# Kernel tuning notes

Measured on AMD Instinct MI355X. Metric: run time of the kernel, lower is better.

Reference implementation:

```python
import jax, jax.numpy as jnp
import numpy as np

D, HEADS, HD, L, P, DFF = 256, 8, 32, 4, 4, 2048
B, NQ = 4, 900
SHAPES = [(128, 128), (64, 64), (32, 32), (16, 16)]
S = sum(h * w for h, w in SHAPES)


def setup_inputs():
    ks = iter(jax.random.split(jax.random.key(0), 20))
    rn = lambda *s: jax.random.normal(next(ks), s, jnp.float32) * 0.02
    cxcy = jax.random.uniform(next(ks), (B, NQ, 1, 2), minval=0.1, maxval=0.9)
    wh = jax.random.uniform(next(ks), (B, NQ, 1, 2), minval=0.05, maxval=0.3)
    ref = jnp.broadcast_to(jnp.concatenate([cxcy, wh], -1), (B, NQ, L, 4))
    starts = np.cumsum([0] + [h * w for h, w in SHAPES[:-1]])
    return dict(
        query=jax.random.normal(next(ks), (B, NQ, D), jnp.float32),
        query_pos=jax.random.normal(next(ks), (B, NQ, D), jnp.float32),
        reference_points=ref,
        input_flatten=jax.random.normal(next(ks), (B, S, D), jnp.float32),
        input_spatial_shapes=jnp.array(SHAPES, jnp.int32),
        input_level_start_index=jnp.array(starts, jnp.int32),
        sa_in_w=rn(3, D, D), sa_in_b=jnp.zeros((3, D)),
        sa_out_w=rn(D, D), sa_out_b=jnp.zeros((D,)),
        norm1_g=jnp.ones((D,)), norm1_b=jnp.zeros((D,)),
        value_w=rn(D, D), value_b=jnp.zeros((D,)),
        off_w=rn(D, HEADS * L * P * 2),
        off_b=jax.random.uniform(next(ks), (HEADS * L * P * 2,), minval=-1.0, maxval=1.0),
        aw_w=rn(D, HEADS * L * P), aw_b=jnp.zeros((HEADS * L * P,)),
        ca_out_w=rn(D, D), ca_out_b=jnp.zeros((D,)),
        norm2_g=jnp.ones((D,)), norm2_b=jnp.zeros((D,)),
        lin1_w=rn(D, DFF), lin1_b=jnp.zeros((DFF,)),
        lin2_w=rn(DFF, D), lin2_b=jnp.zeros((D,)),
        norm3_g=jnp.ones((D,)), norm3_b=jnp.zeros((D,)),
    )


def _ln(x, g, b, eps=1e-5):
    m = x.mean(-1, keepdims=True)
    v = ((x - m) ** 2).mean(-1, keepdims=True)
    return (x - m) * jax.lax.rsqrt(v + eps) * g + b


def _msdeform(q, input_flatten, ref, shapes, starts, value_w, value_b,
              off_w, off_b, aw_w, aw_b, out_w, out_b):
    Bq, Nq, _ = q.shape
    # value: (B, heads, S, head_dim)
    v = (input_flatten @ value_w + value_b).reshape(Bq, -1, HEADS, HD).transpose(0, 2, 1, 3)
    off = (q @ off_w + off_b).reshape(Bq, Nq, HEADS, L, P, 2).transpose(0, 2, 1, 3, 4, 5)
    aw = jax.nn.softmax((q @ aw_w + aw_b).reshape(Bq, Nq, HEADS, L * P), axis=-1)
    aw = aw.reshape(Bq, Nq, HEADS, L, P).transpose(0, 2, 1, 3, 4)  # (B,H,Nq,L,P)
    refc = ref[:, None, :, :, None, :]  # (B,1,Nq,L,1,4)
    # box refs: center + offset/P * wh * 0.5  (Deformable-DETR convention)
    loc = refc[..., :2] + off / P * refc[..., 2:] * 0.5  # (B,H,Nq,L,P,2)
    out = jnp.zeros((Bq, HEADS, Nq, HD), q.dtype)
    for l, (H, W) in enumerate(shapes):
        vl = jax.lax.dynamic_slice_in_dim(v, starts[l], H * W, axis=2)  # (B,H,HW,hd)
        x = loc[:, :, :, l, :, 0] * W - 0.5  # align_corners=False pixel coords
        y = loc[:, :, :, l, :, 1] * H - 0.5
        x0, y0 = jnp.floor(x), jnp.floor(y)
        dx, dy = x - x0, y - y0

        def g(xi, yi):
            valid = (xi >= 0) & (xi < W) & (yi >= 0) & (yi < H)  # zero padding
            idx = (jnp.clip(yi, 0, H - 1) * W + jnp.clip(xi, 0, W - 1)).astype(jnp.int32)
            gat = jnp.take_along_axis(vl, idx.reshape(Bq, HEADS, Nq * P, 1), axis=2)
            return gat.reshape(Bq, HEADS, Nq, P, HD) * valid[..., None]

        samp = (((1 - dx) * (1 - dy))[..., None] * g(x0, y0)
                + (dx * (1 - dy))[..., None] * g(x0 + 1, y0)
                + ((1 - dx) * dy)[..., None] * g(x0, y0 + 1)
                + (dx * dy)[..., None] * g(x0 + 1, y0 + 1))
        out = out + jnp.sum(aw[:, :, :, l, :, None] * samp, axis=3)
    return out.transpose(0, 2, 1, 3).reshape(Bq, Nq, D) @ out_w + out_b


def _layer(query, query_pos, reference_points, input_flatten, shapes, starts, p):
    Bq, Nq, _ = query.shape
    qk = query + query_pos
    heads = lambda x: x.reshape(Bq, Nq, HEADS, HD).transpose(0, 2, 1, 3)
    qh = heads(qk @ p['sa_in_w'][0] + p['sa_in_b'][0])
    kh = heads(qk @ p['sa_in_w'][1] + p['sa_in_b'][1])
    vh = heads(query @ p['sa_in_w'][2] + p['sa_in_b'][2])
    attn = jax.nn.softmax(jnp.einsum('bhqd,bhkd->bhqk', qh, kh) * (HD ** -0.5), axis=-1)
    sa = jnp.einsum('bhqk,bhkd->bhqd', attn, vh).transpose(0, 2, 1, 3).reshape(Bq, Nq, D)
    sa = sa @ p['sa_out_w'] + p['sa_out_b']
    x = _ln(query + sa, p['norm1_g'], p['norm1_b'])
    ca = _msdeform(x + query_pos, input_flatten, reference_points, shapes, starts,
                   p['value_w'], p['value_b'], p['off_w'], p['off_b'],
                   p['aw_w'], p['aw_b'], p['ca_out_w'], p['ca_out_b'])
    x = _ln(x + ca, p['norm2_g'], p['norm2_b'])
    ffn = jax.nn.relu(x @ p['lin1_w'] + p['lin1_b']) @ p['lin2_w'] + p['lin2_b']
    return _ln(x + ffn, p['norm3_g'], p['norm3_b'])


PNAMES = ['sa_in_w', 'sa_in_b', 'sa_out_w', 'sa_out_b', 'norm1_g', 'norm1_b',
          'value_w', 'value_b', 'off_w', 'off_b', 'aw_w', 'aw_b',
          'ca_out_w', 'ca_out_b', 'norm2_g', 'norm2_b',
          'lin1_w', 'lin1_b', 'lin2_w', 'lin2_b', 'norm3_g', 'norm3_b']


def reference(query, query_pos, reference_points, input_flatten,
              input_spatial_shapes, input_level_start_index,
              sa_in_w, sa_in_b, sa_out_w, sa_out_b, norm1_g, norm1_b,
              value_w, value_b, off_w, off_b, aw_w, aw_b,
              ca_out_w, ca_out_b, norm2_g, norm2_b,
              lin1_w, lin1_b, lin2_w, lin2_b, norm3_g, norm3_b):
    # spatial shapes / start indices are static structural metadata
    shapes = [(int(h), int(w)) for h, w in np.asarray(input_spatial_shapes)]
    starts = [int(s) for s in np.asarray(input_level_start_index)]
    p = dict(zip(PNAMES, (sa_in_w, sa_in_b, sa_out_w, sa_out_b, norm1_g, norm1_b,
                          value_w, value_b, off_w, off_b, aw_w, aw_b,
                          ca_out_w, ca_out_b, norm2_g, norm2_b,
                          lin1_w, lin1_b, lin2_w, lin2_b, norm3_g, norm3_b)))
    return _layer(query, query_pos, reference_points, input_flatten, shapes, starts, p)
```

## Files before the change

### kernel.cpp

```cpp
#include <hip/hip_runtime.h>
#include <hip/hip_bf16.h>

#define DD   256
#define NH   8
#define HDIM 32
#define LV   4
#define NP   4
#define DFF  2048
#define BB   4
#define NQQ  900
#define SS   21760

typedef __bf16 bf16x8 __attribute__((ext_vector_type(8)));
typedef __bf16 bf16x2 __attribute__((ext_vector_type(2)));
typedef float  f32x4  __attribute__((ext_vector_type(4)));

__device__ inline void stval(float* p, float v) { *p = v; }
__device__ inline void stval(__bf16* p, float v) { *p = (__bf16)v; }

__device__ __forceinline__ void gload16(const void* g, void* l) {
    __builtin_amdgcn_global_load_lds(
        (const __attribute__((address_space(1))) void*)g,
        (__attribute__((address_space(3))) void*)l, 16, 0, 0);
}

struct TPtrs {
    const float* s[10];
    __bf16* d[10];
};

__global__ void transp_all(TPtrs P) {
    const int Ks[10] = {256, 256, 256, 256, 256, 256, 256, 256, 256, 2048};
    const int Ns[10] = {256, 256, 256, 256, 256, 256, 128, 256, 2048, 256};
    const int tiles[10] = {64, 64, 64, 64, 64, 64, 32, 64, 512, 512};
    int t = blockIdx.x;
    int j = 0, base = 0;
    while (t >= base + tiles[j]) { base += tiles[j]; j++; }
    int lt = t - base;
    int K = Ks[j], N = Ns[j];
    int tn = N >> 5;
    int nb = (lt % tn) * 32, kb = (lt / tn) * 32;
    const float* W = P.s[j];
    __bf16* Wt = P.d[j];
    __shared__ float tbuf[32][33];
    for (int i = threadIdx.y; i < 32; i += 8)
        tbuf[i][threadIdx.x] = W[(size_t)(kb + i) * N + nb + threadIdx.x];
    __syncthreads();
    for (int i = threadIdx.y; i < 32; i += 8)
        Wt[(size_t)(nb + i) * K + kb + threadIdx.x] = (__bf16)tbuf[threadIdx.x][i];
}

#define BM 64
#define BN 64
#define BKK 64

template <typename AT, typename OT, int RELU, int NSUB>
__global__ __launch_bounds__(256) void mfma_gemm(
    const AT* __restrict__ A, const float* __restrict__ A2,
    const __bf16* __restrict__ Wt,
    const float* __restrict__ bias, const float* __restrict__ bias2, int nsplit,
    OT* __restrict__ C, int M, int N, int K) {
    int tid = threadIdx.x;
    int lane = tid & 63;
    int wave = tid >> 6;
    int wr = wave >> 1, wc = wave & 1;
    int m0 = blockIdx.y * BM;
    int n0 = blockIdx.x * (BN * NSUB);

    __shared__ __attribute__((aligned(16))) __bf16 As[BM * BKK];
    __shared__ __attribute__((aligned(16))) __bf16 Bs[NSUB][BN * BKK];

    f32x4 acc[NSUB][2][2] = {};

    int srow = tid >> 2;
    int sq = tid & 3;
    int u0 = sq << 1;
    int p0 = (u0 ^ (srow & 7)) * 8;
    int p1 = ((u0 + 1) ^ (srow & 7)) * 8;
    int fr = lane & 15, gq = lane >> 4;

    for (int k0 = 0; k0 < K; k0 += BKK) {
        {
            int gm = m0 + srow;
            bf16x8 v0 = {}, v1 = {};
            if (gm < M) {
                if constexpr (sizeof(AT) == 4) {
                    const float* ap = (const float*)A + (size_t)gm * K + k0 + sq * 16;
                    f32x4 f0 = *(const f32x4*)(ap + 0);
                    f32x4 f1 = *(const f32x4*)(ap + 4);
                    f32x4 f2 = *(const f32x4*)(ap + 8);
                    f32x4 f3 = *(const f32x4*)(ap + 12);
                    if (A2) {
                        const float* ap2 = A2 + (size_t)gm * K + k0 + sq * 16;
                        f0 += *(const f32x4*)(ap2 + 0);
                        f1 += *(const f32x4*)(ap2 + 4);
                        f2 += *(const f32x4*)(ap2 + 8);
                        f3 += *(const f32x4*)(ap2 + 12);
                    }
#pragma unroll
                    for (int e = 0; e < 4; e++) {
                        v0[e] = (__bf16)f0[e]; v0[e + 4] = (__bf16)f1[e];
                        v1[e] = (__bf16)f2[e]; v1[e + 4] = (__bf16)f3[e];
                    }
                } else {
                    const __bf16* ap = (const __bf16*)A + (size_t)gm * K + k0 + sq * 16;
                    v0 = *(const bf16x8*)(ap);
                    v1 = *(const bf16x8*)(ap + 8);
                }
            }
            *(bf16x8*)(&As[srow * 64 + p0]) = v0;
            *(bf16x8*)(&As[srow * 64 + p1]) = v1;
        }
#pragma unroll
        for (int ns = 0; ns < NSUB; ns++) {
            int gn = n0 + ns * BN + srow;
            const __bf16* bp = Wt + (size_t)gn * K + k0 + sq * 16;
            bf16x8 w0 = *(const bf16x8*)(bp);
            bf16x8 w1 = *(const bf16x8*)(bp + 8);
            *(bf16x8*)(&Bs[ns][srow * 64 + p0]) = w0;
            *(bf16x8*)(&Bs[ns][srow * 64 + p1]) = w1;
        }
        __syncthreads();
#pragma unroll
        for (int ks = 0; ks < 2; ks++) {
            bf16x8 a[2];
#pragma unroll
            for (int i = 0; i < 2; i++) {
                int ma = wr * 32 + i * 16 + fr;
                a[i] = *(const bf16x8*)(&As[ma * 64 + ((ks * 4 + gq) ^ (ma & 7)) * 8]);
            }
#pragma unroll
            for (int ns = 0; ns < NSUB; ns++) {
                bf16x8 b[2];
#pragma unroll
                for (int j = 0; j < 2; j++) {
                    int nb = wc * 32 + j * 16 + fr;
                    b[j] = *(const bf16x8*)(&Bs[ns][nb * 64 + ((ks * 4 + gq) ^ (nb & 7)) * 8]);
                }
#pragma unroll
                for (int i = 0; i < 2; i++)
#pragma unroll
                    for (int j = 0; j < 2; j++)
                        acc[ns][i][j] = __builtin_amdgcn_mfma_f32_16x16x32_bf16(a[i], b[j], acc[ns][i][j], 0, 0, 0);
            }
        }
        __syncthreads();
    }
    int orow = gq * 4;
#pragma unroll
    for (int ns = 0; ns < NSUB; ns++)
#pragma unroll
        for (int i = 0; i < 2; i++)
#pragma unroll
            for (int j = 0; j < 2; j++) {
                int gn = n0 + ns * BN + wc * 32 + j * 16 + fr;
                float bv = (gn < nsplit) ? bias[gn] : bias2[gn - nsplit];
#pragma unroll
                for (int r = 0; r < 4; r++) {
                    int gm = m0 + wr * 32 + i * 16 + orow + r;
                    if (gm < M) {
                        float v = acc[ns][i][j][r] + bv;
                        if (RELU) v = fmaxf(v, 0.f);
                        stval(C + (size_t)gm * N + gn, v);
                    }
                }
            }
}

__global__ __launch_bounds__(256) void value_gemm(
    const float* __restrict__ A, const __bf16* __restrict__ Wt,
    const float* __restrict__ bias, __bf16* __restrict__ C) {
    int tid = threadIdx.x;
    int lane = tid & 63;
    int wave = tid >> 6;
    int wr = wave >> 1, wc = wave & 1;
    int m0 = blockIdx.x * 64;

    __shared__ __attribute__((aligned(16))) __bf16 As[2][64 * 64];
    __shared__ __attribute__((aligned(16))) __bf16 Bs[2][4][64 * 64];

    f32x4 acc[4][2][2] = {};

    int srow = tid >> 2;
    int sq = tid & 3;
    int u0 = sq << 1;
    int p0 = (u0 ^ (srow & 7)) * 8;
    int p1 = ((u0 + 1) ^ (srow & 7)) * 8;
    int fr = lane & 15, gq = lane >> 4;

    int c_row = lane >> 3;
    int c_u = lane & 7;
    int gu = c_u ^ c_row;
    const __bf16* bsrc0 = Wt + (size_t)(wave * 64 + c_row) * 256 + gu * 8;

    const float* aptr = A + (size_t)(m0 + srow) * 256 + sq * 16;

    f32x4 fa0 = *(const f32x4*)(aptr + 0);
    f32x4 fa1 = *(const f32x4*)(aptr + 4);
    f32x4 fa2 = *(const f32x4*)(aptr + 8);
    f32x4 fa3 = *(const f32x4*)(aptr + 12);
#pragma unroll
    for (int c = 0; c < 8; c++)
        gload16(bsrc0 + (size_t)c * 8 * 256, &Bs[0][wave][c * 512]);
    {
        bf16x8 v0, v1;
#pragma unroll
        for (int e = 0; e < 4; e++) {
            v0[e] = (__bf16)fa0[e]; v0[e + 4] = (__bf16)fa1[e];
            v1[e] = (__bf16)fa2[e]; v1[e + 4] = (__bf16)fa3[e];
        }
        *(bf16x8*)(&As[0][srow * 64 + p0]) = v0;
        *(bf16x8*)(&As[0][srow * 64 + p1]) = v1;
    }
    __syncthreads();

    for (int step = 0; step < 4; step++) {
        int p = step & 1;
        if (step < 3) {
            const float* ap2 = aptr + (step + 1) * 64;
            fa0 = *(const f32x4*)(ap2 + 0);
            fa1 = *(const f32x4*)(ap2 + 4);
            fa2 = *(const f32x4*)(ap2 + 8);
            fa3 = *(const f32x4*)(ap2 + 12);
            const __bf16* bsrc = bsrc0 + (step + 1) * 64;
#pragma unroll
            for (int c = 0; c < 8; c++)
                gload16(bsrc + (size_t)c * 8 * 256, &Bs[p ^ 1][wave][c * 512]);
        }
#pragma unroll
        for (int ks = 0; ks < 2; ks++) {
            bf16x8 a[2];
#pragma unroll
            for (int i = 0; i < 2; i++) {
                int ma = wr * 32 + i * 16 + fr;
                a[i] = *(const bf16x8*)(&As[p][ma * 64 + ((ks * 4 + gq) ^ (ma & 7)) * 8]);
            }
#pragma unroll
            for (int ns = 0; ns < 4; ns++) {
                bf16x8 b[2];
#pragma unroll
                for (int j = 0; j < 2; j++) {
                    int nb = wc * 32 + j * 16 + fr;
                    b[j] = *(const bf16x8*)(&Bs[p][ns][nb * 64 + ((ks * 4 + gq) ^ (nb & 7)) * 8]);
                }
#pragma unroll
                for (int i = 0; i < 2; i++)
#pragma unroll
                    for (int j = 0; j < 2; j++)
                        acc[ns][i][j] = __builtin_amdgcn_mfma_f32_16x16x32_bf16(a[i], b[j], acc[ns][i][j], 0, 0, 0);
            }
        }
        if (step < 3) {
            bf16x8 v0, v1;
#pragma unroll
            for (int e = 0; e < 4; e++) {
                v0[e] = (__bf16)fa0[e]; v0[e + 4] = (__bf16)fa1[e];
                v1[e] = (__bf16)fa2[e]; v1[e + 4] = (__bf16)fa3[e];
            }
            *(bf16x8*)(&As[p ^ 1][srow * 64 + p0]) = v0;
            *(bf16x8*)(&As[p ^ 1][srow * 64 + p1]) = v1;
        }
        __syncthreads();
    }

    int orow = gq * 4;
#pragma unroll
    for (int ns = 0; ns < 4; ns++)
#pragma unroll
        for (int i = 0; i < 2; i++)
#pragma unroll
            for (int j = 0; j < 2; j++) {
                int gn = ns * 64 + wc * 32 + j * 16 + fr;
                float bv = bias[gn];
#pragma unroll
                for (int r = 0; r < 4; r++) {
                    int gm = m0 + wr * 32 + i * 16 + orow + r;
                    C[(size_t)gm * 256 + gn] = (__bf16)(acc[ns][i][j][r] + bv);
                }
            }
}

__global__ void fillmark(float* o, int n, float v) {
    int i = blockIdx.x * blockDim.x + threadIdx.x;
    if (i < n) o[i] = v;
}

__global__ void ln_res(const float* a, const float* b,
                       const float* g, const float* be, float* o) {
    int row = blockIdx.x;
    int t = threadIdx.x;
    float x = a[(size_t)row * DD + t] + b[(size_t)row * DD + t];
    __shared__ float red[DD];
    red[t] = x;
    __syncthreads();
    for (int s = 128; s > 0; s >>= 1) {
        if (t < s) red[t] += red[t + s];
        __syncthreads();
    }
    float m = red[0] * (1.f / DD);
    __syncthreads();
    float d0 = x - m;
    red[t] = d0 * d0;
    __syncthreads();
    for (int s = 128; s > 0; s >>= 1) {
        if (t < s) red[t] += red[t + s];
        __syncthreads();
    }
    float v = red[0] * (1.f / DD);
    o[(size_t)row * DD + t] = d0 * rsqrtf(v + 1e-5f) * g[t] + be[t];
}

#define QT 64
#define KT 64
#define NT ((NQQ + KT - 1) / KT)
#define QKLD 512

__global__ __launch_bounds__(256) void sa_attn_mfma(
    const __bf16* __restrict__ QK, const __bf16* __restrict__ V,
    float* __restrict__ O) {
    int blk = blockIdx.x;
    int tq = blk % NT;
    int bh = blk / NT;
    int h = bh % NH;
    int b = bh / NH;
    int tid = threadIdx.x;
    int lane = tid & 63;
    int wave = tid >> 6;
    int fr = lane & 15, gq = lane >> 4;
    int q0 = tq * QT;

    __shared__ __attribute__((aligned(16))) __bf16 Ks[KT][56];
    __shared__ __attribute__((aligned(16))) __bf16 Vt[HDIM][72];
    __shared__ __attribute__((aligned(16))) __bf16 Ps[4][16][72];

    int qrow = q0 + wave * 16 + fr;
    bf16x8 aq = {};
    if (qrow < NQQ)
        aq = *(const bf16x8*)(QK + ((size_t)(b * NQQ + qrow)) * QKLD + h * HDIM + gq * 8);

    f32x4 o0 = {}, o1 = {};
    float m_r[4] = {-1e30f, -1e30f, -1e30f, -1e30f};
    float l_r[4] = {0.f, 0.f, 0.f, 0.f};
    const float scale = 0.17677669529663687f;

    for (int kt = 0; kt < NT; kt++) {
        int kv0 = kt * KT;
        {
            int r = tid >> 2;
            int c8 = (tid & 3) * 8;
            int kvr = kv0 + r;
            bf16x8 kv_ = {}, vv_ = {};
            if (kvr < NQQ) {
                kv_ = *(const bf16x8*)(QK + ((size_t)(b * NQQ + kvr)) * QKLD + 256 + h * HDIM + c8);
                vv_ = *(const bf16x8*)(V + ((size_t)(b * NQQ + kvr)) * DD + h * HDIM + c8);
            }
            *(bf16x8*)(&Ks[r][c8]) = kv_;
#pragma unroll
            for (int j = 0; j < 8; j++) Vt[c8 + j][r] = vv_[j];
        }
        __syncthreads();

        f32x4 s[4];
#pragma unroll
        for (int f = 0; f < 4; f++) {
            bf16x8 bk = *(const bf16x8*)(&Ks[f * 16 + fr][gq * 8]);
            f32x4 z = {};
            s[f] = __builtin_amdgcn_mfma_f32_16x16x32_bf16(aq, bk, z, 0, 0, 0);
        }
#pragma unroll
        for (int f = 0; f < 4; f++) {
            bool valid = (kv0 + f * 16 + fr) < NQQ;
#pragma unroll
            for (int r = 0; r < 4; r++)
                s[f][r] = valid ? s[f][r] * scale : -1e30f;
        }
        float sc_[4];
#pragma unroll
        for (int r = 0; r < 4; r++) {
            float v = fmaxf(fmaxf(s[0][r], s[1][r]), fmaxf(s[2][r], s[3][r]));
            v = fmaxf(v, __shfl_xor(v, 1));
            v = fmaxf(v, __shfl_xor(v, 2));
            v = fmaxf(v, __shfl_xor(v, 4));
            v = fmaxf(v, __shfl_xor(v, 8));
            float mn = fmaxf(m_r[r], v);
            sc_[r] = expf(m_r[r] - mn);
            m_r[r] = mn;
        }
        float rs[4] = {0.f, 0.f, 0.f, 0.f};
#pragma unroll
        for (int f = 0; f < 4; f++)
#pragma unroll
            for (int r = 0; r < 4; r++) {
                float e = expf(s[f][r] - m_r[r]);
                s[f][r] = e;
                rs[r] += e;
            }
#pragma unroll
        for (int r = 0; r < 4; r++) {
            float v = rs[r];
            v += __shfl_xor(v, 1);
            v += __shfl_xor(v, 2);
            v += __shfl_xor(v, 4);
            v += __shfl_xor(v, 8);
            l_r[r] = l_r[r] * sc_[r] + v;
            o0[r] *= sc_[r];
            o1[r] *= sc_[r];
        }
#pragma unroll
        for (int f = 0; f < 4; f++)
#pragma unroll
            for (int r = 0; r < 4; r++)
                Ps[wave][gq * 4 + r][f * 16 + fr] = (__bf16)s[f][r];
#pragma unroll
        for (int c = 0; c < 2; c++) {
            bf16x8 ap = *(const bf16x8*)(&Ps[wave][fr][c * 32 + gq * 8]);
            bf16x8 bv0 = *(const bf16x8*)(&Vt[fr][c * 32 + gq * 8]);
            bf16x8 bv1 = *(const bf16x8*)(&Vt[16 + fr][c * 32 + gq * 8]);
            o0 = __builtin_amdgcn_mfma_f32_16x16x32_bf16(ap, bv0, o0, 0, 0, 0);
            o1 = __builtin_amdgcn_mfma_f32_16x16x32_bf16(ap, bv1, o1, 0, 0, 0);
        }
        __syncthreads();
    }
#pragma unroll
    for (int r = 0; r < 4; r++) {
        int qr = q0 + wave * 16 + gq * 4 + r;
        if (qr < NQQ) {
            float inv = 1.f / l_r[r];
            O[((size_t)(b * NQQ + qr)) * DD + h * HDIM + fr] = o0[r] * inv;
            O[((size_t)(b * NQQ + qr)) * DD + h * HDIM + 16 + fr] = o1[r] * inv;
        }
    }
}

#define OAW 384

__global__ __launch_bounds__(256) void msdeform3(
    const __bf16* __restrict__ val, const __bf16* __restrict__ oa,
    const float* __restrict__ ref, float* __restrict__ out) {
    int tid = threadIdx.x;
    int row = blockIdx.x;
    int b_ = row / NQQ;

    __shared__ float sx[128], sy[128], sw[128];

    if (tid < 128) {
        int h = tid >> 4;
        int lp = tid & 15;
        int l = lp >> 2;
        float logit = (float)oa[(size_t)row * OAW + 256 + h * 16 + lp];
        float ox = (float)oa[(size_t)row * OAW + h * 32 + lp * 2];
        float oy = (float)oa[(size_t)row * OAW + h * 32 + lp * 2 + 1];
        const float* rp = ref + ((size_t)row * LV + l) * 4;
        float cx = rp[0], cy = rp[1], rw = rp[2], rh = rp[3];
        float mv = logit;
        mv = fmaxf(mv, __shfl_xor(mv, 1));
        mv = fmaxf(mv, __shfl_xor(mv, 2));
        mv = fmaxf(mv, __shfl_xor(mv, 4));
        mv = fmaxf(mv, __shfl_xor(mv, 8));
        float e = expf(logit - mv);
        float sum = e;
        sum += __shfl_xor(sum, 1);
        sum += __shfl_xor(sum, 2);
        sum += __shfl_xor(sum, 4);
        sum += __shfl_xor(sum, 8);
        int Wl = 128 >> l;
        float lx = cx + ox * (1.0f / NP) * rw * 0.5f;
        float ly = cy + oy * (1.0f / NP) * rh * 0.5f;
        sx[tid] = lx * Wl - 0.5f;
        sy[tid] = ly * Wl - 0.5f;
        sw[tid] = e / sum;
    }
    __syncthreads();

    int cpar = tid & 7;
    int dgrp = (tid >> 3) & 3;
    int h = tid >> 5;
    const int stt[4] = {0, 16384, 20480, 21504};
    const __bf16* vb = val + (size_t)b_ * SS * DD + h * HDIM + dgrp * 8;
    float facc[8] = {};
#pragma unroll
    for (int k = 0; k < 8; k++) {
        int combo = cpar * 8 + k;
        int lp = combo >> 2;
        int tap = combo & 3;
        int l = lp >> 2;
        int Wl = 128 >> l;
        int cidx = h * 16 + lp;
        float x = sx[cidx], y = sy[cidx], w = sw[cidx];
        float x0f = floorf(x), y0f = floorf(y);
        float dx = x - x0f, dy = y - y0f;
        int xi = (int)x0f + (tap & 1);
        int yi = (int)y0f + (tap >> 1);
        float wt = ((tap & 1) ? dx : 1.f - dx) * ((tap >> 1) ? dy : 1.f - dy) * w;
        if ((xi >= 0) & (xi < Wl) & (yi >= 0) & (yi < Wl)) {
            bf16x8 t = *(const bf16x8*)(vb + (size_t)(stt[l] + yi * Wl + xi) * DD);
#pragma unroll
            for (int e = 0; e < 8; e++) facc[e] += wt * (float)t[e];
        }
    }
#pragma unroll
    for (int e = 0; e < 8; e++) {
        facc[e] += __shfl_xor(facc[e], 1);
        facc[e] += __shfl_xor(facc[e], 2);
        facc[e] += __shfl_xor(facc[e], 4);
    }
    float v = facc[0];
#pragma unroll
    for (int e = 1; e < 8; e++) if (cpar == e) v = facc[e];
    out[(size_t)row * DD + tid] = v;
}

extern "C" void kernel_launch(void* const* d_in, const int* in_sizes, int n_in,
                              void* d_out, int out_size, void* d_ws, size_t ws_size,
                              hipStream_t stream) {
    const float* query      = (const float*)d_in[0];
    const float* query_pos  = (const float*)d_in[1];
    const float* refpts     = (const float*)d_in[2];
    const float* input_flat = (const float*)d_in[3];
    const float* sa_in_w    = (const float*)d_in[6];
    const float* sa_in_b    = (const float*)d_in[7];
    const float* sa_out_w   = (const float*)d_in[8];
    const float* sa_out_b   = (const float*)d_in[9];
    const float* norm1_g    = (const float*)d_in[10];
    const float* norm1_b    = (const float*)d_in[11];
    const float* value_w    = (const float*)d_in[12];
    const float* value_b    = (const float*)d_in[13];
    const float* off_w      = (const float*)d_in[14];
    const float* off_b      = (const float*)d_in[15];
    const float* aw_w       = (const float*)d_in[16];
    const float* aw_b       = (const float*)d_in[17];
    const float* ca_out_w   = (const float*)d_in[18];
    const float* ca_out_b   = (const float*)d_in[19];
    const float* norm2_g    = (const float*)d_in[20];
    const float* norm2_b    = (const float*)d_in[21];
    const float* lin1_w     = (const float*)d_in[22];
    const float* lin1_b     = (const float*)d_in[23];
    const float* lin2_w     = (const float*)d_in[24];
    const float* lin2_b     = (const float*)d_in[25];
    const float* norm3_g    = (const float*)d_in[26];
    const float* norm3_b    = (const float*)d_in[27];
    float* out = (float*)d_out;

    const int M = BB * NQQ;
    const int NE = M * DD;
    const size_t slotBytes = (size_t)NE * 4;
    const size_t wElems = 6 * 65536 + 32768 + 65536 + 2 * 524288;
    const size_t wBytes = wElems * 2;
    const size_t bigBytes = (size_t)BB * SS * DD * 2;
    const size_t needBytes = 3 * slotBytes + wBytes + bigBytes;
    if (ws_size < needBytes) {
        float mark = 1000.0f + (float)(ws_size >> 20);
        fillmark<<<(out_size + 255) / 256, 256, 0, stream>>>(out, out_size, mark);
        return;
    }

    char* wsb = (char*)d_ws;
    float* s0 = (float*)(wsb);
    float* s1 = (float*)(wsb + slotBytes);
    float* s2 = (float*)(wsb + 2 * slotBytes);
    __bf16* wb = (__bf16*)(wsb + 3 * slotBytes);
    __bf16* vbig = (__bf16*)(wsb + 3 * slotBytes + wBytes);

    __bf16* wt_q   = wb;
    __bf16* wt_k   = wb + 65536;
    __bf16* wt_v   = wb + 131072;
    __bf16* wt_sa  = wb + 196608;
    __bf16* wt_val = wb + 262144;
    __bf16* wt_off = wb + 327680;
    __bf16* wt_aw  = wb + 393216;
    __bf16* wt_ca  = wb + 425984;
    __bf16* wt_l1  = wb + 491520;
    __bf16* wt_l2  = wb + 1015808;

    TPtrs tp;
    tp.s[0] = sa_in_w;          tp.d[0] = wt_q;
    tp.s[1] = sa_in_w + 65536;  tp.d[1] = wt_k;
    tp.s[2] = sa_in_w + 131072; tp.d[2] = wt_v;
    tp.s[3] = sa_out_w;         tp.d[3] = wt_sa;
    tp.s[4] = value_w;          tp.d[4] = wt_val;
    tp.s[5] = off_w;            tp.d[5] = wt_off;
    tp.s[6] = aw_w;             tp.d[6] = wt_aw;
    tp.s[7] = ca_out_w;         tp.d[7] = wt_ca;
    tp.s[8] = lin1_w;           tp.d[8] = wt_l1;
    tp.s[9] = lin2_w;           tp.d[9] = wt_l2;
    transp_all<<<1504, dim3(32, 8), 0, stream>>>(tp);

    __bf16* qkbuf = (__bf16*)s1;
    __bf16* Vp = (__bf16*)s2;
    __bf16* oabuf = (__bf16*)s1;

    const int mt = (M + BM - 1) / BM;
    const int mtv = (BB * SS) / BM;
    const int BIG = 1 << 30;

    mfma_gemm<float, __bf16, 0, 1><<<dim3(8, mt), 256, 0, stream>>>(
        query, query_pos, wt_q, sa_in_b, sa_in_b, BIG, qkbuf, M, 512, DD);
    mfma_gemm<float, __bf16, 0, 1><<<dim3(4, mt), 256, 0, stream>>>(
        query, nullptr, wt_v, sa_in_b + 512, sa_in_b, BIG, Vp, M, DD, DD);
    sa_attn_mfma<<<BB * NH * NT, 256, 0, stream>>>(qkbuf, Vp, s0);
    mfma_gemm<float, float, 0, 1><<<dim3(4, mt), 256, 0, stream>>>(
        s0, nullptr, wt_sa, sa_out_b, sa_out_b, BIG, s1, M, DD, DD);
    ln_res<<<M, DD, 0, stream>>>(query, s1, norm1_g, norm1_b, s2);
    value_gemm<<<mtv, 256, 0, stream>>>(input_flat, wt_val, value_b, vbig);
    mfma_gemm<float, __bf16, 0, 1><<<dim3(6, mt), 256, 0, stream>>>(
        s2, query_pos, wt_off, off_b, aw_b, 256, oabuf, M, OAW, DD);
    msdeform3<<<M, 256, 0, stream>>>(vbig, oabuf, refpts, s0);
    mfma_gemm<float, float, 0, 1><<<dim3(4, mt), 256, 0, stream>>>(
        s0, nullptr, wt_ca, ca_out_b, ca_out_b, BIG, s1, M, DD, DD);
    ln_res<<<M, DD, 0, stream>>>(s2, s1, norm2_g, norm2_b, s1);
    mfma_gemm<float, __bf16, 1, 1><<<dim3(32, mt), 256, 0, stream>>>(
        s1, nullptr, wt_l1, lin1_b, lin1_b, BIG, vbig, M, DFF, DD);
    mfma_gemm<__bf16, float, 0, 1><<<dim3(4, mt), 256, 0, stream>>>(
        vbig, nullptr, wt_l2, lin2_b, lin2_b, BIG, s0, M, DD, DFF);
    ln_res<<<M, DD, 0, stream>>>(s1, s0, norm3_g, norm3_b, out);
}
```

Baseline: 217.0 us.

## Remap value GEMM waves to own full N-slab with manual waitcnt pipelining

The value projection GEMM now gives each wave its own 64-column slab of B and all 64 rows of A, instead of a 2x2 wave grid sweeping four N subtiles. Each wave reads only its own B buffer, so the per-k-step LDS traffic for B fragments drops. __syncthreads is replaced with explicit vmcnt/lgkmcnt waits, s_barrier and sched_barriers, so global_load_lds copies can overlap the MFMAs, and the step loop is fully unrolled. The risks are more register pressure from the 4x4 accumulator and fragment arrays, and fragile hand-counted wait values.

```diff
diff --git a/kernel.cpp b/kernel.cpp
--- a/kernel.cpp
+++ b/kernel.cpp
@@ -167,41 +167,42 @@
             }
 }
 
-__global__ __launch_bounds__(256) void value_gemm(
+__global__ __launch_bounds__(256) void value_gemm4(
     const float* __restrict__ A, const __bf16* __restrict__ Wt,
     const float* __restrict__ bias, __bf16* __restrict__ C) {
     int tid = threadIdx.x;
     int lane = tid & 63;
     int wave = tid >> 6;
-    int wr = wave >> 1, wc = wave & 1;
+    int fr = lane & 15, gq = lane >> 4;
     int m0 = blockIdx.x * 64;
 
     __shared__ __attribute__((aligned(16))) __bf16 As[2][64 * 64];
-    __shared__ __attribute__((aligned(16))) __bf16 Bs[2][4][64 * 64];
-
-    f32x4 acc[4][2][2] = {};
+    __shared__ __attribute__((aligned(16))) __bf16 Bq[2][4][64 * 64];
+
+    f32x4 acc[4][4] = {};
 
     int srow = tid >> 2;
     int sq = tid & 3;
     int u0 = sq << 1;
     int p0 = (u0 ^ (srow & 7)) * 8;
     int p1 = ((u0 + 1) ^ (srow & 7)) * 8;
-    int fr = lane & 15, gq = lane >> 4;
 
     int c_row = lane >> 3;
     int c_u = lane & 7;
     int gu = c_u ^ c_row;
     const __bf16* bsrc0 = Wt + (size_t)(wave * 64 + c_row) * 256 + gu * 8;
-
     const float* aptr = A + (size_t)(m0 + srow) * 256 + sq * 16;
 
     f32x4 fa0 = *(const f32x4*)(aptr + 0);
     f32x4 fa1 = *(const f32x4*)(aptr + 4);
     f32x4 fa2 = *(const f32x4*)(aptr + 8);
     f32x4 fa3 = *(const f32x4*)(aptr + 12);
+    __builtin_amdgcn_sched_barrier(0);
 #pragma unroll
     for (int c = 0; c < 8; c++)
-        gload16(bsrc0 + (size_t)c * 8 * 256, &Bs[0][wave][c * 512]);
+        gload16(bsrc0 + (size_t)c * 8 * 256, &Bq[0][wave][c * 512]);
+    asm volatile("s_waitcnt vmcnt(8)" ::: "memory");
+    __builtin_amdgcn_sched_barrier(0);
     {
         bf16x8 v0, v1;
 #pragma unroll
@@ -212,8 +213,10 @@
         *(bf16x8*)(&As[0][srow * 64 + p0]) = v0;
         *(bf16x8*)(&As[0][srow * 64 + p1]) = v1;
     }
-    __syncthreads();
-
+    asm volatile("s_waitcnt lgkmcnt(0)" ::: "memory");
+    __builtin_amdgcn_s_barrier();
+
+#pragma unroll
     for (int step = 0; step < 4; step++) {
         int p = step & 1;
         if (step < 3) {
@@ -222,35 +225,34 @@
             fa1 = *(const f32x4*)(ap2 + 4);
             fa2 = *(const f32x4*)(ap2 + 8);
             fa3 = *(const f32x4*)(ap2 + 12);
+            __builtin_amdgcn_sched_barrier(0);
             const __bf16* bsrc = bsrc0 + (step + 1) * 64;
 #pragma unroll
             for (int c = 0; c < 8; c++)
-                gload16(bsrc + (size_t)c * 8 * 256, &Bs[p ^ 1][wave][c * 512]);
-        }
+                gload16(bsrc + (size_t)c * 8 * 256, &Bq[p ^ 1][wave][c * 512]);
+            asm volatile("s_waitcnt vmcnt(12)" ::: "memory");
+        } else {
+            asm volatile("s_waitcnt vmcnt(0)" ::: "memory");
+        }
+        __builtin_amdgcn_sched_barrier(0);
 #pragma unroll
         for (int ks = 0; ks < 2; ks++) {
-            bf16x8 a[2];
-#pragma unroll
-            for (int i = 0; i < 2; i++) {
-                int ma = wr * 32 + i * 16 + fr;
+            bf16x8 a[4], b[4];
+#pragma unroll
+            for (int i = 0; i < 4; i++) {
+                int ma = i * 16 + fr;
                 a[i] = *(const bf16x8*)(&As[p][ma * 64 + ((ks * 4 + gq) ^ (ma & 7)) * 8]);
-            }
-#pragma unroll
-            for (int ns = 0; ns < 4; ns++) {
-                bf16x8 b[2];
-#pragma unroll
-                for (int j = 0; j < 2; j++) {
-                    int nb = wc * 32 + j * 16 + fr;
-                    b[j] = *(const bf16x8*)(&Bs[p][ns][nb * 64 + ((ks * 4 + gq) ^ (nb & 7)) * 8]);
-                }
-#pragma unroll
-                for (int i = 0; i < 2; i++)
-#pragma unroll
-                    for (int j = 0; j < 2; j++)
-                        acc[ns][i][j] = __builtin_amdgcn_mfma_f32_16x16x32_bf16(a[i], b[j], acc[ns][i][j], 0, 0, 0);
-            }
+                b[i] = *(const bf16x8*)(&Bq[p][wave][ma * 64 + ((ks * 4 + gq) ^ (ma & 7)) * 8]);
+            }
+#pragma unroll
+            for (int i = 0; i < 4; i++)
+#pragma unroll
+                for (int j = 0; j < 4; j++)
+                    acc[i][j] = __builtin_amdgcn_mfma_f32_16x16x32_bf16(a[i], b[j], acc[i][j], 0, 0, 0);
         }
         if (step < 3) {
+            asm volatile("s_waitcnt vmcnt(8)" ::: "memory");
+            __builtin_amdgcn_sched_barrier(0);
             bf16x8 v0, v1;
 #pragma unroll
             for (int e = 0; e < 4; e++) {
@@ -259,25 +261,23 @@
             }
             *(bf16x8*)(&As[p ^ 1][srow * 64 + p0]) = v0;
             *(bf16x8*)(&As[p ^ 1][srow * 64 + p1]) = v1;
-        }
-        __syncthreads();
-    }
-
-    int orow = gq * 4;
-#pragma unroll
-    for (int ns = 0; ns < 4; ns++)
-#pragma unroll
-        for (int i = 0; i < 2; i++)
-#pragma unroll
-            for (int j = 0; j < 2; j++) {
-                int gn = ns * 64 + wc * 32 + j * 16 + fr;
-                float bv = bias[gn];
-#pragma unroll
-                for (int r = 0; r < 4; r++) {
-                    int gm = m0 + wr * 32 + i * 16 + orow + r;
-                    C[(size_t)gm * 256 + gn] = (__bf16)(acc[ns][i][j][r] + bv);
-                }
-            }
+            asm volatile("s_waitcnt lgkmcnt(0)" ::: "memory");
+            __builtin_amdgcn_s_barrier();
+        }
+    }
+
+#pragma unroll
+    for (int i = 0; i < 4; i++)
+#pragma unroll
+        for (int j = 0; j < 4; j++) {
+            int gn = wave * 64 + j * 16 + fr;
+            float bv = bias[gn];
+#pragma unroll
+            for (int r = 0; r < 4; r++) {
+                int gm = m0 + i * 16 + gq * 4 + r;
+                C[(size_t)gm * 256 + gn] = (__bf16)(acc[i][j][r] + bv);
+            }
+        }
 }
 
 __global__ void fillmark(float* o, int n, float v) {
@@ -590,7 +590,6 @@
     __bf16* oabuf = (__bf16*)s1;
 
     const int mt = (M + BM - 1) / BM;
-    const int mtv = (BB * SS) / BM;
     const int BIG = 1 << 30;
 
     mfma_gemm<float, __bf16, 0, 1><<<dim3(8, mt), 256, 0, stream>>>(
@@ -601,7 +600,7 @@
     mfma_gemm<float, float, 0, 1><<<dim3(4, mt), 256, 0, stream>>>(
         s0, nullptr, wt_sa, sa_out_b, sa_out_b, BIG, s1, M, DD, DD);
     ln_res<<<M, DD, 0, stream>>>(query, s1, norm1_g, norm1_b, s2);
-    value_gemm<<<mtv, 256, 0, stream>>>(input_flat, wt_val, value_b, vbig);
+    value_gemm4<<<(BB * SS) / 64, 256, 0, stream>>>(input_flat, wt_val, value_b, vbig);
     mfma_gemm<float, __bf16, 0, 1><<<dim3(6, mt), 256, 0, stream>>>(
         s2, query_pos, wt_off, off_b, aw_b, 256, oabuf, M, OAW, DD);
     msdeform3<<<M, 256, 0, stream>>>(vbig, oabuf, refpts, s0);
```

Result: faster. 210.1 us (-3.2%).
